# Kernel tuning notes

Hardware: AMD Instinct MI355X
Metric: run time of the kernel (lower is better)

## Reference

```python
import jax, jax.numpy as jnp
import numpy as np

N, E, ND, ED, H, OUT, L, VC = 10000, 160000, 8, 4, 128, 256, 6, 6
HEADS, C = 4, 128  # GATConv: out_channels=128 per head, concat=False -> mean over heads


def _ln(x, g, b, eps=1e-5):
    m = x.mean(-1, keepdims=True)
    v = ((x - m) ** 2).mean(-1, keepdims=True)
    return (x - m) * jax.lax.rsqrt(v + eps) * g + b


def _gat_layer(h, src, dst, e_attr, lw, a_src, a_dst, lew, a_edge, bias):
    # h: [N,H]; e_attr: [Etot,H]; PyG GATConv(heads=4, concat=False, edge_dim=H)
    xh = (h @ lw).reshape(N, HEADS, C)                 # [N,4,128]
    eh = (e_attr @ lew).reshape(-1, HEADS, C)          # [Etot,4,128]
    al_s = jnp.einsum('nhc,hc->nh', xh, a_src)
    al_d = jnp.einsum('nhc,hc->nh', xh, a_dst)
    al_e = jnp.einsum('ehc,hc->eh', eh, a_edge)
    alpha = jax.nn.leaky_relu(al_s[src] + al_d[dst] + al_e, 0.2)  # [Etot,4]
    amax = jax.ops.segment_max(alpha, dst, num_segments=N)
    ex = jnp.exp(alpha - amax[dst])
    den = jax.ops.segment_sum(ex, dst, num_segments=N)
    w = ex / (den[dst] + 1e-16)
    out = jax.ops.segment_sum(xh[src] * w[..., None], dst, num_segments=N)  # [N,4,128]
    return out.mean(axis=1) + bias


def setup_inputs() -> dict:
    key = jax.random.key(0)
    ks = jax.random.split(key, 32)
    s = 0.05
    d = {
        'x': jax.random.normal(ks[0], (N, ND), jnp.float32),
        'edge_index': jax.random.randint(ks[1], (2, E), 0, N),
        'edge_attr': jax.random.uniform(ks[2], (E, ED), jnp.float32),
        'vnf_context': jax.random.normal(ks[3], (1, VC), jnp.float32),
        # node embedding
        'node_w': jax.random.normal(ks[4], (ND, H)) * s, 'node_b': jnp.zeros((H,)),
        # EdgeAttentionLayer
        'ea_proj_w': jax.random.normal(ks[5], (ED, H)) * s, 'ea_proj_b': jnp.zeros((H,)),
        'vnf_w': jax.random.normal(ks[6], (VC, H)) * s, 'vnf_b': jnp.zeros((H,)),
        'att1_w': jax.random.normal(ks[7], (2 * H, H)) * s, 'att1_b': jnp.zeros((H,)),
        'att2_w': jax.random.normal(ks[8], (H, H // 2)) * s, 'att2_b': jnp.zeros((H // 2,)),
        'att3_w': jax.random.normal(ks[9], (H // 2, 1)) * s, 'att3_b': jnp.zeros((1,)),
        # per-layer GATConv params (stacked over L layers)
        'gat_lin_w': jax.random.normal(ks[10], (L, H, HEADS * C)) * s,
        'gat_att_src': jax.random.normal(ks[11], (L, HEADS, C)) * s,
        'gat_att_dst': jax.random.normal(ks[12], (L, HEADS, C)) * s,
        'gat_lin_edge_w': jax.random.normal(ks[13], (L, H, HEADS * C)) * s,
        'gat_att_edge': jax.random.normal(ks[14], (L, HEADS, C)) * s,
        'gat_bias': jnp.zeros((L, C)),
        'ln_scale': jnp.ones((L, H)), 'ln_bias': jnp.zeros((L, H)),
        # output projection
        'out_w': jax.random.normal(ks[15], (H, OUT)) * s, 'out_b': jnp.zeros((OUT,)),
    }
    return d


def reference(x, edge_index, edge_attr, vnf_context, node_w, node_b, ea_proj_w, ea_proj_b,
              vnf_w, vnf_b, att1_w, att1_b, att2_w, att2_b, att3_w, att3_b,
              gat_lin_w, gat_att_src, gat_att_dst, gat_lin_edge_w, gat_att_edge, gat_bias,
              ln_scale, ln_bias, out_w, out_b):
    src, dst = edge_index[0], edge_index[1]
    h = x @ node_w + node_b                                   # [N,128]
    # EdgeAttentionLayer (eval mode, no network_state)
    ef = edge_attr @ ea_proj_w + ea_proj_b                    # [E,128]
    vnf = vnf_context @ vnf_w + vnf_b                         # [1,128]
    comb = jnp.concatenate([ef, jnp.broadcast_to(vnf, (E, H))], axis=-1)
    a = jax.nn.relu(comb @ att1_w + att1_b)
    a = jax.nn.relu(a @ att2_w + att2_b)
    e_gate = jax.nn.sigmoid(a @ att3_w + att3_b)              # [E,1]
    w_edge = ef * e_gate                                      # [E,128]
    # GATConv default add_self_loops=True, fill_value='mean'
    loop = jnp.arange(N)
    src2 = jnp.concatenate([src, loop])
    dst2 = jnp.concatenate([dst, loop])
    e2 = jnp.concatenate([w_edge, jnp.broadcast_to(w_edge.mean(0, keepdims=True), (N, H))], axis=0)
    for l in range(L):
        hc = _gat_layer(h, src2, dst2, e2, gat_lin_w[l], gat_att_src[l], gat_att_dst[l],
                        gat_lin_edge_w[l], gat_att_edge[l], gat_bias[l])
        h = _ln(h + jax.nn.relu(hc), ln_scale[l], ln_bias[l])
    return h @ out_w + out_b                                  # [N,256]
```

## Files before the change

### kernel.cpp

```cpp
#include <hip/hip_runtime.h>
#include <hip/hip_bf16.h>
#include <math.h>

#define Nn 10000
#define Ee 160000
#define ET 170000
#define LL 6

typedef short v8s __attribute__((ext_vector_type(8)));
typedef float v4f __attribute__((ext_vector_type(4)));
typedef float v2f __attribute__((ext_vector_type(2)));

__device__ __forceinline__ unsigned short f2bf(float v) {
    unsigned int b = __float_as_uint(v);
    b += 0x7fffu + ((b >> 16) & 1u);
    return (unsigned short)(b >> 16);
}
__device__ __forceinline__ float bflo(unsigned int u) { return __uint_as_float(u << 16); }
__device__ __forceinline__ float bfhi(unsigned int u) { return __uint_as_float(u & 0xffff0000u); }

__global__ void k_node_embed(const float* __restrict__ x, const float* __restrict__ nw,
                             const float* __restrict__ nb, float* __restrict__ h,
                             unsigned short* __restrict__ hb) {
    int idx = blockIdx.x * 256 + threadIdx.x;
    if (idx >= Nn * 128) return;
    int n = idx >> 7, c = idx & 127;
    const float* xr = x + (size_t)n * 8;
    float acc = nb[c];
#pragma unroll
    for (int k = 0; k < 8; k++) acc += xr[k] * nw[k * 128 + c];
    h[idx] = acc;
    hb[idx] = f2bf(acc);
}

__global__ void k_small(const float* __restrict__ vnfc, const float* __restrict__ vw,
                        const float* __restrict__ vb, const float* __restrict__ eab,
                        const float* __restrict__ a1w, const float* __restrict__ a1b,
                        const float* __restrict__ eaw, float* __restrict__ E1) {
    __shared__ float vr[128];
    __shared__ float sM1[512];
    __shared__ float sd1[128];
    int t = threadIdx.x;
    if (t < 128) {
        float a = vb[t];
#pragma unroll
        for (int k = 0; k < 6; k++) a += vnfc[k] * vw[k * 128 + t];
        vr[t] = a;
    }
    __syncthreads();
    if (t < 128) {
        float a = a1b[t];
        for (int k = 0; k < 128; k++) a += eab[k] * a1w[k * 128 + t];
        for (int k = 0; k < 128; k++) a += vr[k] * a1w[(128 + k) * 128 + t];
        sd1[t] = a;
    }
    {
        int r = t >> 7, j = t & 127;
        float a = 0.f;
        for (int k = 0; k < 128; k++) a += eaw[r * 128 + k] * a1w[k * 128 + j];
        sM1[r * 128 + j] = a;
    }
    __syncthreads();
    if (t < 128) {
        E1[t * 8 + 0] = sM1[t];
        E1[t * 8 + 1] = sM1[128 + t];
        E1[t * 8 + 2] = sM1[256 + t];
        E1[t * 8 + 3] = sM1[384 + t];
        E1[t * 8 + 4] = sd1[t];
        E1[t * 8 + 5] = 0.f; E1[t * 8 + 6] = 0.f; E1[t * 8 + 7] = 0.f;
    }
}

__global__ void k_bmat(const float* __restrict__ glw, const float* __restrict__ gas,
                       const float* __restrict__ gad, const float* __restrict__ glew,
                       const float* __restrict__ gae, float* __restrict__ Bs,
                       float* __restrict__ Bd, float* __restrict__ Be) {
    int idx = blockIdx.x * 256 + threadIdx.x;
    if (idx >= LL * 128 * 4) return;
    int hh = idx & 3, k = (idx >> 2) & 127, l = idx >> 9;
    const float* lwp = glw  + (size_t)l * 65536 + k * 512 + hh * 128;
    const float* lep = glew + (size_t)l * 65536 + k * 512 + hh * 128;
    const float* sp = gas + l * 512 + hh * 128;
    const float* dp = gad + l * 512 + hh * 128;
    const float* ep = gae + l * 512 + hh * 128;
    float s1 = 0, s2 = 0, s3 = 0;
    for (int c = 0; c < 128; c++) {
        float lv = lwp[c];
        s1 += lv * sp[c];
        s2 += lv * dp[c];
        s3 += lep[c] * ep[c];
    }
    Bs[idx] = s1; Bd[idx] = s2; Be[idx] = s3;
}

__global__ void k_wsum(const float* __restrict__ glw, unsigned short* __restrict__ WsumT) {
    int idx = blockIdx.x * 256 + threadIdx.x;
    if (idx >= LL * 128 * 512) return;
    int kk = idx & 511;
    int c = (idx >> 9) & 127;
    int l = idx >> 16;
    float v = 0.25f * glw[(size_t)l * 65536 + (size_t)(kk & 127) * 512 + (kk >> 7) * 128 + c];
    WsumT[(size_t)l * 65536 + (size_t)c * 512 + kk] = f2bf(v);
}

__global__ void k_pb(const float* __restrict__ eaw, const float* __restrict__ eab,
                     const float* __restrict__ Be, float* __restrict__ PB,
                     float* __restrict__ cB) {
    int t = threadIdx.x;
    if (t >= 24) return;
    int l = t >> 2, hh = t & 3;
    const float* bp = Be + l * 512 + hh;
    float s0 = 0, s1 = 0, s2 = 0, s3 = 0, sc = 0;
    for (int k = 0; k < 128; k++) {
        float bv = bp[k * 4];
        s0 += eaw[0 * 128 + k] * bv;
        s1 += eaw[1 * 128 + k] * bv;
        s2 += eaw[2 * 128 + k] * bv;
        s3 += eaw[3 * 128 + k] * bv;
        sc += eab[k] * bv;
    }
    PB[0 * 24 + t] = s0; PB[1 * 24 + t] = s1;
    PB[2 * 24 + t] = s2; PB[3 * 24 + t] = s3;
    cB[t] = sc;
}

__global__ __launch_bounds__(256, 3) void k_edge(
    const float* __restrict__ ea, const float* __restrict__ E1,
    const float* __restrict__ a2w, const float* __restrict__ a2b,
    const float* __restrict__ a3w, const float* __restrict__ a3b,
    const float* __restrict__ PB, const float* __restrict__ cB,
    float* __restrict__ aleT, float* __restrict__ gsum) {
    __shared__ float sw2[128 * 64];
    __shared__ float4 sM[128];
    __shared__ float sD[128];
    __shared__ float prs[4][256];
    __shared__ float gsh[256];
    int t = threadIdx.x;
    int lane = t & 63;
    int p = t >> 6;
    int ps = __builtin_amdgcn_readfirstlane(p);
    for (int z = t; z < 2048; z += 256) ((float4*)sw2)[z] = ((const float4*)a2w)[z];
    if (t < 128) { sM[t] = *(const float4*)(E1 + t * 8); sD[t] = E1[t * 8 + 4]; }
    __syncthreads();
    int eb = blockIdx.x * 256 + lane;
    float4 ev[4];
#pragma unroll
    for (int r = 0; r < 4; r++) ev[r] = *(const float4*)(ea + (size_t)(eb + r * 64) * 4);
    v2f acc[4][8];
#pragma unroll
    for (int j = 0; j < 8; j++) {
        v2f b = {a2b[ps * 16 + 2 * j], a2b[ps * 16 + 2 * j + 1]};
#pragma unroll
        for (int r = 0; r < 4; r++) acc[r][j] = b;
    }
    const float* w2base = sw2 + ps * 16;
    for (int k = 0; k < 128; k++) {
        float4 m = sM[k];
        float dk = sD[k];
        v2f xx[4];
#pragma unroll
        for (int r = 0; r < 4; r++) {
            float xv = fmaxf(dk + ev[r].x * m.x + ev[r].y * m.y + ev[r].z * m.z + ev[r].w * m.w, 0.f);
            xx[r][0] = xv; xx[r][1] = xv;
        }
        const float* w2r = w2base + k * 64;
#pragma unroll
        for (int j4 = 0; j4 < 4; j4++) {
            float4 wv = *(const float4*)(w2r + j4 * 4);
            v2f w01 = {wv.x, wv.y}, w23 = {wv.z, wv.w};
#pragma unroll
            for (int r = 0; r < 4; r++) {
                acc[r][2 * j4]     += xx[r] * w01;
                acc[r][2 * j4 + 1] += xx[r] * w23;
            }
        }
    }
#pragma unroll
    for (int r = 0; r < 4; r++) {
        float pr = 0.f;
#pragma unroll
        for (int j = 0; j < 8; j++) {
            pr += fmaxf(acc[r][j][0], 0.f) * a3w[ps * 16 + 2 * j];
            pr += fmaxf(acc[r][j][1], 0.f) * a3w[ps * 16 + 2 * j + 1];
        }
        prs[p][r * 64 + lane] = pr;
    }
    __syncthreads();
    if (p == 0) {
        float v0 = 0.f, v1 = 0.f, v2 = 0.f, v3 = 0.f, v4 = 0.f;
#pragma unroll
        for (int rep = 0; rep < 4; rep++) {
            int le = rep * 64 + lane;
            float tot = prs[0][le] + prs[1][le] + prs[2][le] + prs[3][le] + a3b[0];
            float g = 1.f / (1.f + __expf(-tot));
            gsh[le] = g;
            float4 evv = ev[rep];
            v0 += g; v1 += g * evv.x; v2 += g * evv.y; v3 += g * evv.z; v4 += g * evv.w;
        }
#pragma unroll
        for (int d = 32; d > 0; d >>= 1) {
            v0 += __shfl_down(v0, d); v1 += __shfl_down(v1, d); v2 += __shfl_down(v2, d);
            v3 += __shfl_down(v3, d); v4 += __shfl_down(v4, d);
        }
        if (lane == 0) {
            atomicAdd(&gsum[0], v0); atomicAdd(&gsum[1], v1); atomicAdd(&gsum[2], v2);
            atomicAdd(&gsum[3], v3); atomicAdd(&gsum[4], v4);
        }
    }
    __syncthreads();
#pragma unroll
    for (int rep = 0; rep < 2; rep++) {
        int i4 = (rep == 0) ? ps : (ps < 2 ? ps + 4 : -1);
        if (i4 >= 0) {
            float4 c  = *(const float4*)(cB + i4 * 4);
            float4 p0 = *(const float4*)(PB + 0 * 24 + i4 * 4);
            float4 p1 = *(const float4*)(PB + 1 * 24 + i4 * 4);
            float4 p2 = *(const float4*)(PB + 2 * 24 + i4 * 4);
            float4 p3 = *(const float4*)(PB + 3 * 24 + i4 * 4);
#pragma unroll
            for (int r = 0; r < 4; r++) {
                float g = gsh[r * 64 + lane];
                float4 evv = ev[r];
                float4 o;
                o.x = g * (c.x + evv.x * p0.x + evv.y * p1.x + evv.z * p2.x + evv.w * p3.x);
                o.y = g * (c.y + evv.x * p0.y + evv.y * p1.y + evv.z * p2.y + evv.w * p3.y);
                o.z = g * (c.z + evv.x * p0.z + evv.y * p1.z + evv.z * p2.z + evv.w * p3.z);
                o.w = g * (c.w + evv.x * p0.w + evv.y * p1.w + evv.z * p2.w + evv.w * p3.w);
                *(float4*)(aleT + (size_t)i4 * Ee * 4 + (size_t)(eb + r * 64) * 4) = o;
            }
        }
    }
}

__global__ void k_lale(const float* __restrict__ gsum, const float* __restrict__ PB,
                       const float* __restrict__ cB, float* __restrict__ lale) {
    int t = threadIdx.x;
    if (t >= 24) return;
    float s = gsum[0] * cB[t] + gsum[1] * PB[t] + gsum[2] * PB[24 + t]
            + gsum[3] * PB[48 + t] + gsum[4] * PB[72 + t];
    lale[t] = s * (1.0f / Ee);
}

__global__ void k_hist(const int* __restrict__ ei, int* __restrict__ hist) {
    int i = blockIdx.x * 256 + threadIdx.x;
    if (i >= ET) return;
    int d = (i < Ee) ? ei[Ee + i] : (i - Ee);
    atomicAdd(&hist[d], 1);
}

__global__ __launch_bounds__(1024) void k_scan(const int* __restrict__ hist,
                                               int* __restrict__ seg, int* __restrict__ pos) {
    __shared__ int wsums[16];
    __shared__ int carry_s;
    int t = threadIdx.x;
    int lane = t & 63, wid = t >> 6;
    if (t == 0) { carry_s = 0; seg[0] = 0; }
    __syncthreads();
    for (int base = 0; base < Nn; base += 1024) {
        int idx = base + t;
        int v = (idx < Nn) ? hist[idx] : 0;
        int sc = v;
#pragma unroll
        for (int d = 1; d < 64; d <<= 1) {
            int up = __shfl_up(sc, d);
            if (lane >= d) sc += up;
        }
        if (lane == 63) wsums[wid] = sc;
        __syncthreads();
        if (wid == 0) {
            int wv = (lane < 16) ? wsums[lane] : 0;
            int wsc = wv;
#pragma unroll
            for (int d = 1; d < 16; d <<= 1) {
                int up = __shfl_up(wsc, d);
                if (lane >= d) wsc += up;
            }
            if (lane < 16) wsums[lane] = wsc - wv;
        }
        __syncthreads();
        int carry = carry_s;
        int inc = sc + wsums[wid] + carry;
        if (idx < Nn) { seg[idx + 1] = inc; pos[idx] = inc - v; }
        __syncthreads();
        if (t == 1023) carry_s = inc;
        __syncthreads();
    }
}

__global__ void k_scatter(const int* __restrict__ ei, int* __restrict__ pos,
                          int2* __restrict__ pse) {
    int i = blockIdx.x * 256 + threadIdx.x;
    if (i >= ET) return;
    int s, d;
    if (i < Ee) { s = ei[i]; d = ei[Ee + i]; } else { s = d = i - Ee; }
    int idx = atomicAdd(&pos[d], 1);
    pse[idx] = make_int2(s, i);
}

__global__ void k_ab(const float* __restrict__ h, const float* __restrict__ Bs_l,
                     const float* __restrict__ Bd_l, float* __restrict__ als,
                     float* __restrict__ ald) {
    int idx = blockIdx.x * 256 + threadIdx.x;
    if (idx >= Nn * 8) return;
    int n = idx >> 3, slot = idx & 7;
    const float* B = (slot < 4) ? Bs_l : Bd_l;
    int hh = slot & 3;
    const float4* hr = (const float4*)(h + (size_t)n * 128);
    float s = 0.f;
#pragma unroll 8
    for (int kb = 0; kb < 32; kb++) {
        float4 hv = hr[kb];
        s += hv.x * B[(4 * kb + 0) * 4 + hh] + hv.y * B[(4 * kb + 1) * 4 + hh]
           + hv.z * B[(4 * kb + 2) * 4 + hh] + hv.w * B[(4 * kb + 3) * 4 + hh];
    }
    if (slot < 4) als[n * 4 + hh] = s;
    else          ald[n * 4 + hh] = s;
}

__global__ __launch_bounds__(256) void k_agg3(
    const int2* __restrict__ pse, const int* __restrict__ seg,
    const float* __restrict__ als, const float* __restrict__ ald,
    const float* __restrict__ aleT_l, const float* __restrict__ lale_l,
    const unsigned short* __restrict__ hb, unsigned short* __restrict__ aggb) {
    __shared__ float part[2][512];
    __shared__ float pden[2][4];
    int t = threadIdx.x;
    int lane = t & 63;
    int wv = (t >> 6) & 1;
    int w = t >> 7;
    int n = blockIdx.x * 2 + w;
    int start = seg[n], end = seg[n + 1];
    int deg = end - start;
    int half = (deg + 1) >> 1;
    int s0 = start + wv * half;
    int e0 = wv ? end : start + half;
    int hp = lane >> 4;
    int cch = (lane & 15) * 8;
    float aldh = ald[n * 4 + hp];
    float llh = lale_l[hp];
    float den = 0.f;
    float4 acc0 = make_float4(0.f, 0.f, 0.f, 0.f);
    float4 acc1 = make_float4(0.f, 0.f, 0.f, 0.f);
    int i = s0;
    for (; i + 2 <= e0; i += 2) {
        int2 sa = pse[i], sb = pse[i + 1];
        float ala = sa.y < Ee ? aleT_l[(size_t)sa.y * 4 + hp] : llh;
        float alb = sb.y < Ee ? aleT_l[(size_t)sb.y * 4 + hp] : llh;
        float ava = als[sa.x * 4 + hp] + aldh + ala;
        float avb = als[sb.x * 4 + hp] + aldh + alb;
        ava = ava > 0.f ? ava : 0.2f * ava;
        avb = avb > 0.f ? avb : 0.2f * avb;
        float ea = __expf(fminf(ava, 60.f));
        float eb = __expf(fminf(avb, 60.f));
        den += ea + eb;
        uint4 ua = *(const uint4*)(hb + (size_t)sa.x * 128 + cch);
        uint4 ub = *(const uint4*)(hb + (size_t)sb.x * 128 + cch);
        acc0.x += ea * bflo(ua.x) + eb * bflo(ub.x);
        acc0.y += ea * bfhi(ua.x) + eb * bfhi(ub.x);
        acc0.z += ea * bflo(ua.y) + eb * bflo(ub.y);
        acc0.w += ea * bfhi(ua.y) + eb * bfhi(ub.y);
        acc1.x += ea * bflo(ua.z) + eb * bflo(ub.z);
        acc1.y += ea * bfhi(ua.z) + eb * bfhi(ub.z);
        acc1.z += ea * bflo(ua.w) + eb * bflo(ub.w);
        acc1.w += ea * bfhi(ua.w) + eb * bfhi(ub.w);
    }
    if (i < e0) {
        int2 sa = pse[i];
        float ala = sa.y < Ee ? aleT_l[(size_t)sa.y * 4 + hp] : llh;
        float ava = als[sa.x * 4 + hp] + aldh + ala;
        ava = ava > 0.f ? ava : 0.2f * ava;
        float ea = __expf(fminf(ava, 60.f));
        den += ea;
        uint4 ua = *(const uint4*)(hb + (size_t)sa.x * 128 + cch);
        acc0.x += ea * bflo(ua.x); acc0.y += ea * bfhi(ua.x);
        acc0.z += ea * bflo(ua.y); acc0.w += ea * bfhi(ua.y);
        acc1.x += ea * bflo(ua.z); acc1.y += ea * bfhi(ua.z);
        acc1.z += ea * bflo(ua.w); acc1.w += ea * bfhi(ua.w);
    }
    if (wv == 1) {
        *(float4*)&part[w][lane * 8] = acc0;
        *(float4*)&part[w][lane * 8 + 4] = acc1;
        if ((lane & 15) == 0) pden[w][hp] = den;
    }
    __syncthreads();
    if (wv == 0) {
        float4 p0 = *(const float4*)&part[w][lane * 8];
        float4 p1 = *(const float4*)&part[w][lane * 8 + 4];
        float inv = 1.f / (den + pden[w][hp] + 1e-16f);
        acc0.x = (acc0.x + p0.x) * inv; acc0.y = (acc0.y + p0.y) * inv;
        acc0.z = (acc0.z + p0.z) * inv; acc0.w = (acc0.w + p0.w) * inv;
        acc1.x = (acc1.x + p1.x) * inv; acc1.y = (acc1.y + p1.y) * inv;
        acc1.z = (acc1.z + p1.z) * inv; acc1.w = (acc1.w + p1.w) * inv;
        ushort4 q0, q1;
        q0.x = f2bf(acc0.x); q0.y = f2bf(acc0.y); q0.z = f2bf(acc0.z); q0.w = f2bf(acc0.w);
        q1.x = f2bf(acc1.x); q1.y = f2bf(acc1.y); q1.z = f2bf(acc1.z); q1.w = f2bf(acc1.w);
        *(ushort4*)(aggb + (size_t)n * 512 + lane * 8) = q0;
        *(ushort4*)(aggb + (size_t)n * 512 + lane * 8 + 4) = q1;
    }
}

__global__ __launch_bounds__(256) void k_post(
    const unsigned short* __restrict__ aggb, const unsigned short* __restrict__ WsumT_l,
    const float* __restrict__ gbias, const float* __restrict__ lnsc,
    const float* __restrict__ lnbi, float* __restrict__ h,
    unsigned short* __restrict__ hb, const float* __restrict__ Bs_n,
    const float* __restrict__ Bd_n, float* __restrict__ als, float* __restrict__ ald) {
    int t = threadIdx.x;
    int lane = t & 63, w = t >> 6;
    int n0 = (blockIdx.x * 4 + w) * 16;
    if (n0 >= Nn) return;
    int m = lane & 15, q = lane >> 4;
    v4f acc[8];
#pragma unroll
    for (int nt = 0; nt < 8; nt++) acc[nt] = (v4f){0.f, 0.f, 0.f, 0.f};
    const unsigned short* arow = aggb + (size_t)(n0 + m) * 512 + q * 8;
#pragma unroll 4
    for (int ks = 0; ks < 16; ks++) {
        v8s fa = *(const v8s*)(arow + ks * 32);
#pragma unroll
        for (int nt = 0; nt < 8; nt++) {
            int col = nt * 16 + m;
            v8s fb = *(const v8s*)(WsumT_l + (size_t)col * 512 + ks * 32 + q * 8);
            acc[nt] = __builtin_amdgcn_mfma_f32_16x16x32_bf16(fa, fb, acc[nt], 0, 0, 0);
        }
    }
    float v[8][4];
    float s1[4] = {0.f, 0.f, 0.f, 0.f}, s2[4] = {0.f, 0.f, 0.f, 0.f};
#pragma unroll
    for (int nt = 0; nt < 8; nt++) {
        int col = nt * 16 + m;
        float b = gbias[col];
#pragma unroll
        for (int r = 0; r < 4; r++) {
            int row = n0 + q * 4 + r;
            float val = h[(size_t)row * 128 + col] + fmaxf(acc[nt][r] + b, 0.f);
            v[nt][r] = val;
            s1[r] += val; s2[r] += val * val;
        }
    }
#pragma unroll
    for (int d = 1; d <= 8; d <<= 1) {
#pragma unroll
        for (int r = 0; r < 4; r++) {
            s1[r] += __shfl_xor(s1[r], d);
            s2[r] += __shfl_xor(s2[r], d);
        }
    }
    float o8[8][4];
#pragma unroll
    for (int r = 0; r < 4; r++) {
        float mean = s1[r] * (1.f / 128.f);
        float var = s2[r] * (1.f / 128.f) - mean * mean;
        float rinv = rsqrtf(var + 1e-5f);
        int row = n0 + q * 4 + r;
#pragma unroll
        for (int nt = 0; nt < 8; nt++) {
            int col = nt * 16 + m;
            float o = (v[nt][r] - mean) * rinv * lnsc[col] + lnbi[col];
            o8[nt][r] = o;
            h[(size_t)row * 128 + col] = o;
            hb[(size_t)row * 128 + col] = f2bf(o);
        }
    }
    float sal[4][4], sad[4][4];
#pragma unroll
    for (int r = 0; r < 4; r++) {
#pragma unroll
        for (int hh = 0; hh < 4; hh++) { sal[r][hh] = 0.f; sad[r][hh] = 0.f; }
    }
#pragma unroll
    for (int nt = 0; nt < 8; nt++) {
        int col = nt * 16 + m;
        float4 bs = *(const float4*)(Bs_n + col * 4);
        float4 bd = *(const float4*)(Bd_n + col * 4);
#pragma unroll
        for (int r = 0; r < 4; r++) {
            float o = o8[nt][r];
            sal[r][0] += o * bs.x; sal[r][1] += o * bs.y;
            sal[r][2] += o * bs.z; sal[r][3] += o * bs.w;
            sad[r][0] += o * bd.x; sad[r][1] += o * bd.y;
            sad[r][2] += o * bd.z; sad[r][3] += o * bd.w;
        }
    }
#pragma unroll
    for (int d = 1; d <= 8; d <<= 1) {
#pragma unroll
        for (int r = 0; r < 4; r++) {
#pragma unroll
            for (int hh = 0; hh < 4; hh++) {
                sal[r][hh] += __shfl_xor(sal[r][hh], d);
                sad[r][hh] += __shfl_xor(sad[r][hh], d);
            }
        }
    }
    if (m < 8) {
        int hh = m & 3;
#pragma unroll
        for (int r = 0; r < 4; r++) {
            int row = n0 + q * 4 + r;
            float va = (hh == 0) ? sal[r][0] : (hh == 1) ? sal[r][1] : (hh == 2) ? sal[r][2] : sal[r][3];
            float vd = (hh == 0) ? sad[r][0] : (hh == 1) ? sad[r][1] : (hh == 2) ? sad[r][2] : sad[r][3];
            if (m < 4) als[row * 4 + hh] = va;
            else       ald[row * 4 + hh] = vd;
        }
    }
}

__global__ __launch_bounds__(256) void k_out(
    const float* __restrict__ h, const float* __restrict__ ow,
    const float* __restrict__ ob, float* __restrict__ out) {
    __shared__ float4 hs4[8][32];
    int t = threadIdx.x;
    int n0 = blockIdx.x * 8;
    if (t < 256) {
        int i = t >> 5, kb = t & 31;
        hs4[i][kb] = *(const float4*)(h + (size_t)(n0 + i) * 128 + 4 * kb);
    }
    __syncthreads();
    float acc[8] = {0, 0, 0, 0, 0, 0, 0, 0};
    for (int kb = 0; kb < 32; kb++) {
        float w0 = ow[(4 * kb + 0) * 256 + t];
        float w1 = ow[(4 * kb + 1) * 256 + t];
        float w2 = ow[(4 * kb + 2) * 256 + t];
        float w3 = ow[(4 * kb + 3) * 256 + t];
#pragma unroll
        for (int i = 0; i < 8; i++) {
            float4 hv = hs4[i][kb];
            acc[i] += hv.x * w0 + hv.y * w1 + hv.z * w2 + hv.w * w3;
        }
    }
    float b = ob[t];
#pragma unroll
    for (int i = 0; i < 8; i++) out[(size_t)(n0 + i) * 256 + t] = acc[i] + b;
}

extern "C" void kernel_launch(void* const* d_in, const int* in_sizes, int n_in,
                              void* d_out, int out_size, void* d_ws, size_t ws_size,
                              hipStream_t stream) {
    const float* x    = (const float*)d_in[0];
    const int*   ei   = (const int*)d_in[1];
    const float* ea   = (const float*)d_in[2];
    const float* vnfc = (const float*)d_in[3];
    const float* nw   = (const float*)d_in[4];
    const float* nb   = (const float*)d_in[5];
    const float* eaw  = (const float*)d_in[6];
    const float* eab  = (const float*)d_in[7];
    const float* vw   = (const float*)d_in[8];
    const float* vb   = (const float*)d_in[9];
    const float* a1w  = (const float*)d_in[10];
    const float* a1b  = (const float*)d_in[11];
    const float* a2w  = (const float*)d_in[12];
    const float* a2b  = (const float*)d_in[13];
    const float* a3w  = (const float*)d_in[14];
    const float* a3b  = (const float*)d_in[15];
    const float* glw  = (const float*)d_in[16];
    const float* gas  = (const float*)d_in[17];
    const float* gad  = (const float*)d_in[18];
    const float* glew = (const float*)d_in[19];
    const float* gae  = (const float*)d_in[20];
    const float* gb   = (const float*)d_in[21];
    const float* lnsc = (const float*)d_in[22];
    const float* lnbi = (const float*)d_in[23];
    const float* ow   = (const float*)d_in[24];
    const float* ob   = (const float*)d_in[25];
    float* out = (float*)d_out;

    char* w = (char*)d_ws;
    size_t o = 0;
    auto allocf = [&](size_t cnt) { float* p = (float*)(w + o); o += ((cnt * 4 + 255) / 256) * 256; return p; };
    auto alloci = [&](size_t cnt) { int* p = (int*)(w + o); o += ((cnt * 4 + 255) / 256) * 256; return p; };
    auto allocu = [&](size_t cnt) { unsigned short* p = (unsigned short*)(w + o); o += ((cnt * 2 + 255) / 256) * 256; return p; };
    float* h      = allocf((size_t)Nn * 128);
    unsigned short* hb    = allocu((size_t)Nn * 128);
    unsigned short* aggb  = allocu((size_t)Nn * 512);
    unsigned short* WsumT = allocu((size_t)LL * 128 * 512);
    float* als    = allocf((size_t)Nn * 4);
    float* ald    = allocf((size_t)Nn * 4);
    float* aleT   = allocf((size_t)LL * Ee * 4);
    float* Bs     = allocf(3072);
    float* Bd     = allocf(3072);
    float* Be     = allocf(3072);
    float* E1     = allocf(1024);
    float* PB     = allocf(96);
    float* cB     = allocf(24);
    float* gsum   = allocf(8);
    float* lale   = allocf(32);
    int* seg  = alloci(Nn + 1);
    int* hist = alloci(Nn);
    int* pos  = alloci(Nn);
    int2* pse = (int2*)alloci((size_t)ET * 2);

    hipMemsetAsync(hist, 0, Nn * sizeof(int), stream);
    hipMemsetAsync(gsum, 0, 8 * sizeof(float), stream);

    k_node_embed<<<(Nn * 128 + 255) / 256, 256, 0, stream>>>(x, nw, nb, h, hb);
    k_small<<<1, 512, 0, stream>>>(vnfc, vw, vb, eab, a1w, a1b, eaw, E1);
    k_bmat<<<(LL * 128 * 4 + 255) / 256, 256, 0, stream>>>(glw, gas, gad, glew, gae, Bs, Bd, Be);
    k_wsum<<<(LL * 128 * 512 + 255) / 256, 256, 0, stream>>>(glw, WsumT);
    k_pb<<<1, 32, 0, stream>>>(eaw, eab, Be, PB, cB);
    k_edge<<<Ee / 256, 256, 0, stream>>>(ea, E1, a2w, a2b, a3w, a3b, PB, cB, aleT, gsum);
    k_hist<<<(ET + 255) / 256, 256, 0, stream>>>(ei, hist);
    k_scan<<<1, 1024, 0, stream>>>(hist, seg, pos);
    k_scatter<<<(ET + 255) / 256, 256, 0, stream>>>(ei, pos, pse);
    k_lale<<<1, 32, 0, stream>>>(gsum, PB, cB, lale);
    k_ab<<<(Nn * 8 + 255) / 256, 256, 0, stream>>>(h, Bs, Bd, als, ald);
    for (int l = 0; l < LL; l++) {
        int ln = (l + 1) % LL;
        k_agg3<<<Nn / 2, 256, 0, stream>>>(pse, seg, als, ald, aleT + (size_t)l * Ee * 4,
                                           lale + l * 4, hb, aggb);
        k_post<<<(625 + 3) / 4, 256, 0, stream>>>(aggb, WsumT + (size_t)l * 65536,
                                                  gb + l * 128, lnsc + l * 128, lnbi + l * 128,
                                                  h, hb, Bs + ln * 512, Bd + ln * 512, als, ald);
    }
    k_out<<<Nn / 8, 256, 0, stream>>>(h, ow, ob, out);
}
```

Before: 559.6 us.

## Recompute edge attention logits in aggregation from CSR-permuted gated edge features

Instead of precomputing per-layer edge logits (6 layers × 160k edges × 4 heads floats) in k_edge, stores only the gate and gated edge features (5 floats per edge), permutes them into destination-sorted order once, and recomputes the per-head edge logit in k_agg3 from the small PB/cB tables. This removes a large write of precomputed logits and turns the random per-edge gathers in the aggregation into contiguous reads. The cost is a little extra arithmetic per edge in each layer plus a new permutation kernel. Self-loop entries use the mean gated features, which matches the previous mean-based logit because the map is linear.

```diff
diff --git a/kernel.cpp b/kernel.cpp
--- a/kernel.cpp
+++ b/kernel.cpp
@@ -128,8 +128,7 @@
     const float* __restrict__ ea, const float* __restrict__ E1,
     const float* __restrict__ a2w, const float* __restrict__ a2b,
     const float* __restrict__ a3w, const float* __restrict__ a3b,
-    const float* __restrict__ PB, const float* __restrict__ cB,
-    float* __restrict__ aleT, float* __restrict__ gsum) {
+    float* __restrict__ Gg, float4* __restrict__ Ge4, float* __restrict__ gsum) {
     __shared__ float sw2[128 * 64];
     __shared__ float4 sM[128];
     __shared__ float sD[128];
@@ -208,37 +207,13 @@
         }
     }
     __syncthreads();
-#pragma unroll
-    for (int rep = 0; rep < 2; rep++) {
-        int i4 = (rep == 0) ? ps : (ps < 2 ? ps + 4 : -1);
-        if (i4 >= 0) {
-            float4 c  = *(const float4*)(cB + i4 * 4);
-            float4 p0 = *(const float4*)(PB + 0 * 24 + i4 * 4);
-            float4 p1 = *(const float4*)(PB + 1 * 24 + i4 * 4);
-            float4 p2 = *(const float4*)(PB + 2 * 24 + i4 * 4);
-            float4 p3 = *(const float4*)(PB + 3 * 24 + i4 * 4);
-#pragma unroll
-            for (int r = 0; r < 4; r++) {
-                float g = gsh[r * 64 + lane];
-                float4 evv = ev[r];
-                float4 o;
-                o.x = g * (c.x + evv.x * p0.x + evv.y * p1.x + evv.z * p2.x + evv.w * p3.x);
-                o.y = g * (c.y + evv.x * p0.y + evv.y * p1.y + evv.z * p2.y + evv.w * p3.y);
-                o.z = g * (c.z + evv.x * p0.z + evv.y * p1.z + evv.z * p2.z + evv.w * p3.z);
-                o.w = g * (c.w + evv.x * p0.w + evv.y * p1.w + evv.z * p2.w + evv.w * p3.w);
-                *(float4*)(aleT + (size_t)i4 * Ee * 4 + (size_t)(eb + r * 64) * 4) = o;
-            }
-        }
-    }
-}
-
-__global__ void k_lale(const float* __restrict__ gsum, const float* __restrict__ PB,
-                       const float* __restrict__ cB, float* __restrict__ lale) {
-    int t = threadIdx.x;
-    if (t >= 24) return;
-    float s = gsum[0] * cB[t] + gsum[1] * PB[t] + gsum[2] * PB[24 + t]
-            + gsum[3] * PB[48 + t] + gsum[4] * PB[72 + t];
-    lale[t] = s * (1.0f / Ee);
+    {
+        int e = blockIdx.x * 256 + ps * 64 + lane;
+        float g = gsh[ps * 64 + lane];
+        float4 evv = *(const float4*)(ea + (size_t)e * 4);
+        Gg[e] = g;
+        Ge4[e] = make_float4(g * evv.x, g * evv.y, g * evv.z, g * evv.w);
+    }
 }
 
 __global__ void k_hist(const int* __restrict__ ei, int* __restrict__ hist) {
@@ -295,6 +270,22 @@
     if (i < Ee) { s = ei[i]; d = ei[Ee + i]; } else { s = d = i - Ee; }
     int idx = atomicAdd(&pos[d], 1);
     pse[idx] = make_int2(s, i);
+}
+
+__global__ void k_gperm(const int2* __restrict__ pse, const float* __restrict__ Gg,
+                        const float4* __restrict__ Ge4, const float* __restrict__ gsum,
+                        float* __restrict__ Gsg, float4* __restrict__ Gse) {
+    int i = blockIdx.x * 256 + threadIdx.x;
+    if (i >= ET) return;
+    int y = pse[i].y;
+    if (y < Ee) {
+        Gsg[i] = Gg[y];
+        Gse[i] = Ge4[y];
+    } else {
+        float inv = 1.f / Ee;
+        Gsg[i] = gsum[0] * inv;
+        Gse[i] = make_float4(gsum[1] * inv, gsum[2] * inv, gsum[3] * inv, gsum[4] * inv);
+    }
 }
 
 __global__ void k_ab(const float* __restrict__ h, const float* __restrict__ Bs_l,
@@ -320,7 +311,8 @@
 __global__ __launch_bounds__(256) void k_agg3(
     const int2* __restrict__ pse, const int* __restrict__ seg,
     const float* __restrict__ als, const float* __restrict__ ald,
-    const float* __restrict__ aleT_l, const float* __restrict__ lale_l,
+    const float* __restrict__ Gsg, const float4* __restrict__ Gse,
+    const float* __restrict__ PB, const float* __restrict__ cB, int l,
     const unsigned short* __restrict__ hb, unsigned short* __restrict__ aggb) {
     __shared__ float part[2][512];
     __shared__ float pden[2][4];
@@ -337,24 +329,30 @@
     int hp = lane >> 4;
     int cch = (lane & 15) * 8;
     float aldh = ald[n * 4 + hp];
-    float llh = lale_l[hp];
+    float c0 = cB[l * 4 + hp];
+    float pc0 = PB[0 * 24 + l * 4 + hp];
+    float pc1 = PB[1 * 24 + l * 4 + hp];
+    float pc2 = PB[2 * 24 + l * 4 + hp];
+    float pc3 = PB[3 * 24 + l * 4 + hp];
     float den = 0.f;
     float4 acc0 = make_float4(0.f, 0.f, 0.f, 0.f);
     float4 acc1 = make_float4(0.f, 0.f, 0.f, 0.f);
     int i = s0;
     for (; i + 2 <= e0; i += 2) {
-        int2 sa = pse[i], sb = pse[i + 1];
-        float ala = sa.y < Ee ? aleT_l[(size_t)sa.y * 4 + hp] : llh;
-        float alb = sb.y < Ee ? aleT_l[(size_t)sb.y * 4 + hp] : llh;
-        float ava = als[sa.x * 4 + hp] + aldh + ala;
-        float avb = als[sb.x * 4 + hp] + aldh + alb;
+        int sa = pse[i].x, sb = pse[i + 1].x;
+        float ga = Gsg[i], gbv = Gsg[i + 1];
+        float4 ga4 = Gse[i], gb4 = Gse[i + 1];
+        float ala = ga * c0 + ga4.x * pc0 + ga4.y * pc1 + ga4.z * pc2 + ga4.w * pc3;
+        float alb = gbv * c0 + gb4.x * pc0 + gb4.y * pc1 + gb4.z * pc2 + gb4.w * pc3;
+        float ava = als[sa * 4 + hp] + aldh + ala;
+        float avb = als[sb * 4 + hp] + aldh + alb;
         ava = ava > 0.f ? ava : 0.2f * ava;
         avb = avb > 0.f ? avb : 0.2f * avb;
         float ea = __expf(fminf(ava, 60.f));
         float eb = __expf(fminf(avb, 60.f));
         den += ea + eb;
-        uint4 ua = *(const uint4*)(hb + (size_t)sa.x * 128 + cch);
-        uint4 ub = *(const uint4*)(hb + (size_t)sb.x * 128 + cch);
+        uint4 ua = *(const uint4*)(hb + (size_t)sa * 128 + cch);
+        uint4 ub = *(const uint4*)(hb + (size_t)sb * 128 + cch);
         acc0.x += ea * bflo(ua.x) + eb * bflo(ub.x);
         acc0.y += ea * bfhi(ua.x) + eb * bfhi(ub.x);
         acc0.z += ea * bflo(ua.y) + eb * bflo(ub.y);
@@ -365,13 +363,15 @@
         acc1.w += ea * bfhi(ua.w) + eb * bfhi(ub.w);
     }
     if (i < e0) {
-        int2 sa = pse[i];
-        float ala = sa.y < Ee ? aleT_l[(size_t)sa.y * 4 + hp] : llh;
-        float ava = als[sa.x * 4 + hp] + aldh + ala;
+        int sa = pse[i].x;
+        float ga = Gsg[i];
+        float4 ga4 = Gse[i];
+        float ala = ga * c0 + ga4.x * pc0 + ga4.y * pc1 + ga4.z * pc2 + ga4.w * pc3;
+        float ava = als[sa * 4 + hp] + aldh + ala;
         ava = ava > 0.f ? ava : 0.2f * ava;
         float ea = __expf(fminf(ava, 60.f));
         den += ea;
-        uint4 ua = *(const uint4*)(hb + (size_t)sa.x * 128 + cch);
+        uint4 ua = *(const uint4*)(hb + (size_t)sa * 128 + cch);
         acc0.x += ea * bflo(ua.x); acc0.y += ea * bfhi(ua.x);
         acc0.z += ea * bflo(ua.y); acc0.w += ea * bfhi(ua.y);
         acc1.x += ea * bflo(ua.z); acc1.y += ea * bfhi(ua.z);
@@ -576,7 +576,10 @@
     unsigned short* WsumT = allocu((size_t)LL * 128 * 512);
     float* als    = allocf((size_t)Nn * 4);
     float* ald    = allocf((size_t)Nn * 4);
-    float* aleT   = allocf((size_t)LL * Ee * 4);
+    float* Gg     = allocf((size_t)Ee);
+    float4* Ge4   = (float4*)allocf((size_t)Ee * 4);
+    float* Gsg    = allocf((size_t)ET);
+    float4* Gse   = (float4*)allocf((size_t)ET * 4);
     float* Bs     = allocf(3072);
     float* Bd     = allocf(3072);
     float* Be     = allocf(3072);
@@ -584,7 +587,6 @@
     float* PB     = allocf(96);
     float* cB     = allocf(24);
     float* gsum   = allocf(8);
-    float* lale   = allocf(32);
     int* seg  = alloci(Nn + 1);
     int* hist = alloci(Nn);
     int* pos  = alloci(Nn);
@@ -598,16 +600,15 @@
     k_bmat<<<(LL * 128 * 4 + 255) / 256, 256, 0, stream>>>(glw, gas, gad, glew, gae, Bs, Bd, Be);
     k_wsum<<<(LL * 128 * 512 + 255) / 256, 256, 0, stream>>>(glw, WsumT);
     k_pb<<<1, 32, 0, stream>>>(eaw, eab, Be, PB, cB);
-    k_edge<<<Ee / 256, 256, 0, stream>>>(ea, E1, a2w, a2b, a3w, a3b, PB, cB, aleT, gsum);
+    k_edge<<<Ee / 256, 256, 0, stream>>>(ea, E1, a2w, a2b, a3w, a3b, Gg, Ge4, gsum);
     k_hist<<<(ET + 255) / 256, 256, 0, stream>>>(ei, hist);
     k_scan<<<1, 1024, 0, stream>>>(hist, seg, pos);
     k_scatter<<<(ET + 255) / 256, 256, 0, stream>>>(ei, pos, pse);
-    k_lale<<<1, 32, 0, stream>>>(gsum, PB, cB, lale);
+    k_gperm<<<(ET + 255) / 256, 256, 0, stream>>>(pse, Gg, Ge4, gsum, Gsg, Gse);
     k_ab<<<(Nn * 8 + 255) / 256, 256, 0, stream>>>(h, Bs, Bd, als, ald);
     for (int l = 0; l < LL; l++) {
         int ln = (l + 1) % LL;
-        k_agg3<<<Nn / 2, 256, 0, stream>>>(pse, seg, als, ald, aleT + (size_t)l * Ee * 4,
-                                           lale + l * 4, hb, aggb);
+        k_agg3<<<Nn / 2, 256, 0, stream>>>(pse, seg, als, ald, Gsg, Gse, PB, cB, l, hb, aggb);
         k_post<<<(625 + 3) / 4, 256, 0, stream>>>(aggb, WsumT + (size_t)l * 65536,
                                                   gb + l * 128, lnsc + l * 128, lnbi + l * 128,
                                                   h, hb, Bs + ln * 512, Bd + ln * 512, als, ald);
```

After: 574.5 us. 2.7% more time.
